# Kernel tuning notes

Measured on AMD Instinct MI355X. Metric: run time of the kernel, lower is better.

## Reference

```python
import jax, jax.numpy as jnp
import numpy as np
import math

EMBED_DIM = 768
NUM_HEADS = 12
MLP_HIDDEN = int(EMBED_DIM * 2.0)
LN_EPS = 1e-6


def _complex_linear(r, i, wr, wi, br, bi):
    # (r + i*j) @ (wr + wi*j)^T + (br + bi*j)
    out_r = r @ wr.T - i @ wi.T + br
    out_i = r @ wi.T + i @ wr.T + bi
    return out_r, out_i


def _complex_layernorm(r, i, gamma, beta):
    # magnitude-based LN over feature dim; gamma/beta: [F, 2]
    mag = jnp.sqrt(r * r + i * i + LN_EPS)           # [..., F]
    mean = mag.mean(axis=-1, keepdims=True)
    var = ((mag - mean) ** 2).mean(axis=-1, keepdims=True)  # unbiased=False
    norm_mag = (mag - mean) / jnp.sqrt(var + LN_EPS)
    scale = norm_mag / (mag + LN_EPS)
    r_n = r * scale
    i_n = i * scale
    return gamma[..., 0] * r_n + beta[..., 0], gamma[..., 1] * i_n + beta[..., 1]


def setup_inputs() -> dict:
    key = jax.random.key(0)
    ks = jax.random.split(key, 12)
    B, N, E, H = 2, 2048, EMBED_DIM, MLP_HIDDEN
    std_qkv = math.sqrt(2.0 / (E + 3 * E))
    std_proj = math.sqrt(2.0 / (E + E))
    std_fc1 = math.sqrt(2.0 / (E + H))
    std_fc2 = math.sqrt(2.0 / (H + E))
    inp = {
        "x": jax.random.normal(ks[0], (B, N, 2 * E), dtype=jnp.float32),
        "norm1_gamma": 1.0 + 0.1 * jax.random.normal(ks[1], (E, 2), dtype=jnp.float32),
        "norm1_beta": 0.1 * jax.random.normal(ks[2], (E, 2), dtype=jnp.float32),
        "qkv_wr": std_qkv * jax.random.normal(ks[3], (3 * E, E), dtype=jnp.float32),
        "qkv_wi": std_qkv * jax.random.normal(ks[4], (3 * E, E), dtype=jnp.float32),
        "qkv_br": jnp.zeros((3 * E,), dtype=jnp.float32),
        "qkv_bi": jnp.zeros((3 * E,), dtype=jnp.float32),
        "proj_wr": std_proj * jax.random.normal(ks[5], (E, E), dtype=jnp.float32),
        "proj_wi": std_proj * jax.random.normal(ks[6], (E, E), dtype=jnp.float32),
        "proj_br": jnp.zeros((E,), dtype=jnp.float32),
        "proj_bi": jnp.zeros((E,), dtype=jnp.float32),
        "norm2_gamma": 1.0 + 0.1 * jax.random.normal(ks[7], (E, 2), dtype=jnp.float32),
        "norm2_beta": 0.1 * jax.random.normal(ks[8], (E, 2), dtype=jnp.float32),
        "fc1_wr": std_fc1 * jax.random.normal(ks[9], (H, E), dtype=jnp.float32),
        "fc1_wi": std_fc1 * jax.random.normal(ks[10], (H, E), dtype=jnp.float32),
        "fc1_br": jnp.zeros((H,), dtype=jnp.float32),
        "fc1_bi": jnp.zeros((H,), dtype=jnp.float32),
        "fc2_wr": std_fc2 * jax.random.normal(ks[11], (E, H), dtype=jnp.float32),
        "fc2_wi": std_fc2 * jax.random.normal(jax.random.fold_in(key, 99), (E, H), dtype=jnp.float32),
        "fc2_br": jnp.zeros((E,), dtype=jnp.float32),
        "fc2_bi": jnp.zeros((E,), dtype=jnp.float32),
    }
    return inp


def reference(x, norm1_gamma, norm1_beta, qkv_wr, qkv_wi, qkv_br, qkv_bi,
              proj_wr, proj_wi, proj_br, proj_bi, norm2_gamma, norm2_beta,
              fc1_wr, fc1_wi, fc1_br, fc1_bi, fc2_wr, fc2_wi, fc2_br, fc2_bi):
    B, N, _ = x.shape
    E, nH = EMBED_DIM, NUM_HEADS
    hd = E // nH
    xc = x.reshape(B, N, E, 2)
    xr, xi = xc[..., 0], xc[..., 1]

    # --- attention branch ---
    nr, ni = _complex_layernorm(xr, xi, norm1_gamma, norm1_beta)
    qkv_r, qkv_i = _complex_linear(nr, ni, qkv_wr, qkv_wi, qkv_br, qkv_bi)  # [B,N,3E]
    # split to [3, B, nH, N, hd]
    def split_heads(t):
        return t.reshape(B, N, 3, nH, hd).transpose(2, 0, 3, 1, 4)
    qkv_r = split_heads(qkv_r)
    qkv_i = split_heads(qkv_i)
    qr, kr, vr = qkv_r[0], qkv_r[1], qkv_r[2]
    qi, ki, vi = qkv_i[0], qkv_i[1], qkv_i[2]

    # complex attention scores: q * conj-free formulation per source
    attn_real = jnp.einsum('bhqd,bhkd->bhqk', qr, kr) + jnp.einsum('bhqd,bhkd->bhqk', qi, ki)
    attn_imag = jnp.einsum('bhqd,bhkd->bhqk', qr, ki) - jnp.einsum('bhqd,bhkd->bhqk', qi, kr)
    attn_mag = jnp.sqrt(attn_real ** 2 + attn_imag ** 2 + 1e-8) / math.sqrt(hd)
    attn_w = jax.nn.softmax(attn_mag, axis=-1)
    out_r = jnp.einsum('bhqk,bhkd->bhqd', attn_w, vr)
    out_i = jnp.einsum('bhqk,bhkd->bhqd', attn_w, vi)
    # [B,nH,N,hd] -> [B,N,E]
    out_r = out_r.transpose(0, 2, 1, 3).reshape(B, N, E)
    out_i = out_i.transpose(0, 2, 1, 3).reshape(B, N, E)
    pr, pi = _complex_linear(out_r, out_i, proj_wr, proj_wi, proj_br, proj_bi)
    xr = xr + pr
    xi = xi + pi

    # --- MLP branch ---
    nr2, ni2 = _complex_layernorm(xr, xi, norm2_gamma, norm2_beta)
    h_r, h_i = _complex_linear(nr2, ni2, fc1_wr, fc1_wi, fc1_br, fc1_bi)
    h_r = jax.nn.gelu(h_r, approximate=False)
    h_i = jax.nn.gelu(h_i, approximate=False)
    m_r, m_i = _complex_linear(h_r, h_i, fc2_wr, fc2_wi, fc2_br, fc2_bi)
    xr = xr + m_r
    xi = xi + m_i

    return jnp.stack([xr, xi], axis=-1).reshape(B, N, 2 * E)
```

## Files before the change

### kernel.cpp

```cpp
#include <hip/hip_runtime.h>
#include <cmath>

typedef __bf16 bf16;
typedef __bf16 bf16x8 __attribute__((ext_vector_type(8)));
typedef __bf16 bf16x4 __attribute__((ext_vector_type(4)));
typedef float  f32x4  __attribute__((ext_vector_type(4)));
typedef unsigned int u32x4 __attribute__((ext_vector_type(4)));

#define MFMA16(a, b, c) __builtin_amdgcn_mfma_f32_16x16x32_bf16((a), (b), (c), 0, 0, 0)
#define LOG2E 1.44269504088896f

static __device__ __forceinline__ void gl_lds16(const void* g, void* l) {
    __builtin_amdgcn_global_load_lds((const __attribute__((address_space(1))) void*)g,
                                     (__attribute__((address_space(3))) void*)l, 16, 0, 0);
}

static __device__ __forceinline__ bf16x8 bneg8(bf16x8 x) {
    u32x4 u = __builtin_bit_cast(u32x4, x);
    u = u ^ 0x80008000u;
    return __builtin_bit_cast(bf16x8, u);
}

static __device__ __forceinline__ f32x4 zero4() {
    return f32x4{0.0f, 0.0f, 0.0f, 0.0f};
}

__global__ void fill_kernel(float* p, float v, int n) {
    for (int i = blockIdx.x * blockDim.x + threadIdx.x; i < n; i += gridDim.x * blockDim.x)
        p[i] = v;
}

struct Cvt8 {
    const float* s[8];
    bf16* d[8];
    int boff[9];
};
__global__ __launch_bounds__(256) void cvt8_kernel(Cvt8 c) {
    int blk = blockIdx.x;
    int seg = 0;
#pragma unroll
    for (int k = 0; k < 7; ++k)
        if (blk >= c.boff[k + 1]) seg = k + 1;
    const int local = blk - c.boff[seg];
    const int i = local * 1024 + threadIdx.x * 4;
    const float4 v = *(const float4*)(c.s[seg] + i);
    bf16x4 o;
    o[0] = (bf16)v.x; o[1] = (bf16)v.y; o[2] = (bf16)v.z; o[3] = (bf16)v.w;
    *(bf16x4*)(c.d[seg] + i) = o;
}

template <bool ILV>
__global__ __launch_bounds__(256) void cln_kernel(
    const float* __restrict__ xa, const float* __restrict__ xb,
    const float* __restrict__ gamma, const float* __restrict__ beta,
    bf16* __restrict__ nr, bf16* __restrict__ ni) {
    __shared__ float red[4];
    const int t = threadIdx.x;
    const size_t base = (size_t)blockIdx.x * 768;

    float r[3], im[3], mg[3];
#pragma unroll
    for (int j = 0; j < 3; ++j) {
        const int f = t + j * 256;
        if (ILV) {
            const float2 v = ((const float2*)xa)[base + f];
            r[j] = v.x;
            im[j] = v.y;
        } else {
            r[j] = xa[base + f];
            im[j] = xb[base + f];
        }
        mg[j] = __builtin_amdgcn_sqrtf(r[j] * r[j] + im[j] * im[j] + 1e-6f);
    }
    float s = mg[0] + mg[1] + mg[2];
#pragma unroll
    for (int m = 32; m >= 1; m >>= 1) s += __shfl_xor(s, m);
    if ((t & 63) == 0) red[t >> 6] = s;
    __syncthreads();
    const float mean = (red[0] + red[1] + red[2] + red[3]) * (1.0f / 768.0f);
    __syncthreads();

    float v2 = 0.0f;
#pragma unroll
    for (int j = 0; j < 3; ++j) {
        const float d = mg[j] - mean;
        v2 += d * d;
    }
#pragma unroll
    for (int m = 32; m >= 1; m >>= 1) v2 += __shfl_xor(v2, m);
    if ((t & 63) == 0) red[t >> 6] = v2;
    __syncthreads();
    const float var = (red[0] + red[1] + red[2] + red[3]) * (1.0f / 768.0f);
    const float rstd = rsqrtf(var + 1e-6f);

#pragma unroll
    for (int j = 0; j < 3; ++j) {
        const int f = t + j * 256;
        const float sc = (mg[j] - mean) * rstd / (mg[j] + 1e-6f);
        nr[base + f] = (bf16)(gamma[2 * f] * (r[j] * sc) + beta[2 * f]);
        ni[base + f] = (bf16)(gamma[2 * f + 1] * (im[j] * sc) + beta[2 * f + 1]);
    }
}

template <int BM, int BN, int MODE, int OCC>
__global__ __launch_bounds__(256, OCC) void cgemm_kernel(
    const bf16* __restrict__ Ar, const bf16* __restrict__ Ai,
    const bf16* __restrict__ Wr, const bf16* __restrict__ Wi,
    const float* __restrict__ br, const float* __restrict__ bi,
    const float* __restrict__ resr, const float* __restrict__ resi,
    float* __restrict__ outFr, float* __restrict__ outFi,
    bf16* __restrict__ outBr, bf16* __restrict__ outBi,
    int N, int K) {
    constexpr int MR = BM / 32;
    constexpr int NR = BN / 32;
    constexpr int ASEG = BM / 8;
    constexpr int NSEG = (BM + BN) / 8;
    constexpr int SPW = NSEG / 4;

    __shared__ __align__(16) bf16 sA[2][BM][64];
    __shared__ __align__(16) bf16 sB[2][BN][64];

    const int tid = threadIdx.x;
    const int wave = tid >> 6, lane = tid & 63;
    const int lg = lane >> 4, lr = lane & 15;

    const int nwgx = gridDim.x;
    int wg = blockIdx.y * nwgx + blockIdx.x;
    const int cpx = (nwgx * gridDim.y) >> 3;
    wg = (wg & 7) * cpx + (wg >> 3);
    const int row0 = (wg % nwgx) * BM, col0 = (wg / nwgx) * BN;

    const int wm = (wave >> 1) * (BM / 2), wn = (wave & 1) * (BN / 2);

    const int srow = lane >> 3;
    const int schunk = (lane & 7) ^ srow;
    const int spl = schunk >> 2;
    const int sc8 = (schunk & 3) * 8;

    auto issue = [&](int buf, int kt) {
#pragma unroll
        for (int s = 0; s < SPW; ++s) {
            const int id = wave * SPW + s;
            if (id < ASEG) {
                const int row = id * 8 + srow;
                gl_lds16((spl ? Ai : Ar) + (size_t)(row0 + row) * K + kt + sc8,
                         &sA[buf][id * 8][0]);
            } else {
                const int row = (id - ASEG) * 8 + srow;
                gl_lds16((spl ? Wi : Wr) + (size_t)(col0 + row) * K + kt + sc8,
                         &sB[buf][(id - ASEG) * 8][0]);
            }
        }
    };

    f32x4 accr[MR][NR], acci[MR][NR];
#pragma unroll
    for (int a = 0; a < MR; ++a)
#pragma unroll
        for (int b2 = 0; b2 < NR; ++b2) {
            accr[a][b2] = zero4();
            acci[a][b2] = zero4();
        }

    issue(0, 0);

    const int KT = K / 32;
    for (int kt = 0; kt < KT; ++kt) {
        const int buf = kt & 1;
        if (kt + 1 < KT) {
            issue(buf ^ 1, (kt + 1) * 32);
            __builtin_amdgcn_sched_barrier(0);
            if constexpr (SPW == 8)
                asm volatile("s_waitcnt vmcnt(8)" ::: "memory");
            else if constexpr (SPW == 6)
                asm volatile("s_waitcnt vmcnt(6)" ::: "memory");
            else
                asm volatile("s_waitcnt vmcnt(0)" ::: "memory");
        } else {
            asm volatile("s_waitcnt vmcnt(0)" ::: "memory");
        }
        __builtin_amdgcn_sched_barrier(0);
        __builtin_amdgcn_s_barrier();
        __builtin_amdgcn_sched_barrier(0);

        bf16x8 ar[MR], ai[MR], an[MR];
#pragma unroll
        for (int mt = 0; mt < MR; ++mt) {
            const int rr = wm + mt * 16 + lr;
            const int slr = lg ^ (rr & 7);
            const int sli = (4 + lg) ^ (rr & 7);
            ar[mt] = *(const bf16x8*)(&sA[buf][rr][slr * 8]);
            ai[mt] = *(const bf16x8*)(&sA[buf][rr][sli * 8]);
            an[mt] = bneg8(ai[mt]);
        }
#pragma unroll
        for (int nt = 0; nt < NR; ++nt) {
            const int rr = wn + nt * 16 + lr;
            const int slr = lg ^ (rr & 7);
            const int sli = (4 + lg) ^ (rr & 7);
            const bf16x8 br8 = *(const bf16x8*)(&sB[buf][rr][slr * 8]);
            const bf16x8 bi8 = *(const bf16x8*)(&sB[buf][rr][sli * 8]);
#pragma unroll
            for (int mt = 0; mt < MR; ++mt) {
                accr[mt][nt] = MFMA16(ar[mt], br8, accr[mt][nt]);
                accr[mt][nt] = MFMA16(an[mt], bi8, accr[mt][nt]);
                acci[mt][nt] = MFMA16(ar[mt], bi8, acci[mt][nt]);
                acci[mt][nt] = MFMA16(ai[mt], br8, acci[mt][nt]);
            }
        }
    }

#pragma unroll
    for (int nt = 0; nt < NR; ++nt) {
        const int col = col0 + wn + nt * 16 + lr;
        const float bre = br[col], bie = bi[col];
#pragma unroll
        for (int mt = 0; mt < MR; ++mt) {
#pragma unroll
            for (int j = 0; j < 4; ++j) {
                const int row = row0 + wm + mt * 16 + lg * 4 + j;
                float vr = accr[mt][nt][j] + bre;
                float vi = acci[mt][nt][j] + bie;
                const size_t o = (size_t)row * N + col;
                if (MODE == 0) {
                    outBr[o] = (bf16)vr;
                    outBi[o] = (bf16)vi;
                } else if (MODE == 1) {
                    const float2 rv = ((const float2*)resr)[(size_t)row * 768 + col];
                    outFr[o] = rv.x + vr;
                    outFi[o] = rv.y + vi;
                } else if (MODE == 2) {
                    const float t2r = fmaf(vr * vr, 0.044715f, 1.0f);
                    const float er = __builtin_amdgcn_exp2f(vr * t2r * 2.3022082f);
                    vr = vr - vr * __builtin_amdgcn_rcpf(er + 1.0f);
                    const float t2i = fmaf(vi * vi, 0.044715f, 1.0f);
                    const float ei = __builtin_amdgcn_exp2f(vi * t2i * 2.3022082f);
                    vi = vi - vi * __builtin_amdgcn_rcpf(ei + 1.0f);
                    outBr[o] = (bf16)vr;
                    outBi[o] = (bf16)vi;
                } else {
                    const size_t ro = (size_t)row * 768 + col;
                    outFr[(size_t)row * 1536 + 2 * col]     = resr[ro] + vr;
                    outFr[(size_t)row * 1536 + 2 * col + 1] = resi[ro] + vi;
                }
            }
        }
    }
}

__global__ __launch_bounds__(256) void vtrans_kernel(
    const bf16* __restrict__ qkvr, const bf16* __restrict__ qkvi,
    bf16* __restrict__ vtr, bf16* __restrict__ vti) {
    __shared__ bf16 sr[64][65];
    __shared__ bf16 si[64][65];
    const int t = threadIdx.x;
    const int nb = blockIdx.x, h = blockIdx.y, b = blockIdx.z;
    const size_t ld = 2304;
    const bf16* srcr = qkvr + (size_t)(b * 2048 + nb * 64) * ld + 1536 + h * 64;
    const bf16* srci = qkvi + (size_t)(b * 2048 + nb * 64) * ld + 1536 + h * 64;
#pragma unroll
    for (int j = 0; j < 16; ++j) {
        const int idx = t + 256 * j;
        const int n = idx >> 6, d = idx & 63;
        sr[n][d] = srcr[(size_t)n * ld + d];
        si[n][d] = srci[(size_t)n * ld + d];
    }
    __syncthreads();
    bf16* dstr = vtr + (size_t)(b * 12 + h) * 64 * 2048 + nb * 64;
    bf16* dsti = vti + (size_t)(b * 12 + h) * 64 * 2048 + nb * 64;
#pragma unroll
    for (int j = 0; j < 16; ++j) {
        const int idx = t + 256 * j;
        const int d = idx >> 6, n = idx & 63;
        dstr[(size_t)d * 2048 + n] = sr[n][d];
        dsti[(size_t)d * 2048 + n] = si[n][d];
    }
}

__global__ __launch_bounds__(256, 3) void cattn_kernel(
    const bf16* __restrict__ qkvr, const bf16* __restrict__ qkvi,
    const bf16* __restrict__ vtr, const bf16* __restrict__ vti,
    bf16* __restrict__ aor, bf16* __restrict__ aoi) {
    __shared__ __align__(16) bf16 sK[2][2][32][64];
    __shared__ __align__(16) bf16 sV[3][64][64];
    __shared__ __align__(16) bf16 sP[4][16][40];

    const int tid = threadIdx.x;
    const int w = tid >> 6, lane = tid & 63;
    const int lg = lane >> 4, lr = lane & 15;
    const int qb = blockIdx.x, h = blockIdx.y, b = blockIdx.z;
    const int ld = 2304;

    const int s_krow = lane >> 3;
    const int s_kch8 = ((lane & 7) ^ s_krow) * 8;
    const int s_vlog = (lane & 7) ^ s_krow;
    const int s_vpl = s_vlog >> 2;
    const int s_vk8 = (s_vlog & 3) * 8;

    const bf16* kbase0 = qkvr + (size_t)b * 2048 * ld + 768 + h * 64;
    const bf16* kbase1 = qkvi + (size_t)b * 2048 * ld + 768 + h * 64;
    const bf16* vbase = (s_vpl ? vti : vtr) + (size_t)(b * 12 + h) * 64 * 2048;

    const bf16* kp0 = kbase0 + (size_t)(w * 8 + s_krow) * ld + s_kch8;
    const bf16* kp1 = kbase1 + (size_t)(w * 8 + s_krow) * ld + s_kch8;
    const bf16* vp0 = vbase + (size_t)(w * 8 + s_krow) * 2048 + s_vk8;
    const bf16* vp1 = vbase + (size_t)((4 + w) * 8 + s_krow) * 2048 + s_vk8;

    auto stage = [&](int kb, int vs) {
        gl_lds16(kp0, &sK[kb][0][w * 8][0]);
        gl_lds16(kp1, &sK[kb][1][w * 8][0]);
        gl_lds16(vp0, &sV[vs][w * 8][0]);
        gl_lds16(vp1, &sV[vs][(4 + w) * 8][0]);
        kp0 += 32 * ld;
        kp1 += 32 * ld;
        vp0 += 32;
        vp1 += 32;
    };

    stage(0, 0);

    const size_t qoff = (size_t)(b * 2048 + qb * 64 + w * 16 + lr) * ld + h * 64;
    bf16x8 aqr[2], aqi[2];
#pragma unroll
    for (int ks = 0; ks < 2; ++ks) {
        aqr[ks] = *(const bf16x8*)(qkvr + qoff + ks * 32 + lg * 8);
        aqi[ks] = *(const bf16x8*)(qkvi + qoff + ks * 32 + lg * 8);
    }

    f32x4 our[4], oui[4];
#pragma unroll
    for (int d = 0; d < 4; ++d) {
        our[d] = zero4();
        oui[d] = zero4();
    }
    const float C1 = 0.125f * LOG2E;
    float mrun = -1e30f;
    float lrun_p = 0.0f;
    float thr2 = -1.0f;
    float mC2 = 0.0f;

    bf16x8 pfPrev = __builtin_bit_cast(bf16x8, u32x4{0u, 0u, 0u, 0u});
    int vcur = 0, vlast = 0;
    const int slr = lg ^ (lr & 7);
    const int sli = (4 + lg) ^ (lr & 7);

    for (int kt = 0; kt < 64; ++kt) {
        const int kcur = kt & 1;
        int vnext = vcur + 1;
        if (vnext == 3) vnext = 0;
        if (kt < 63) {
            stage(kcur ^ 1, vnext);
            __builtin_amdgcn_sched_barrier(0);
            asm volatile("s_waitcnt vmcnt(4)" ::: "memory");
        } else {
            asm volatile("s_waitcnt vmcnt(0)" ::: "memory");
        }
        __builtin_amdgcn_sched_barrier(0);
        __builtin_amdgcn_s_barrier();
        __builtin_amdgcn_sched_barrier(0);

        f32x4 str[2], sti[2];
        str[0] = zero4(); str[1] = zero4();
        sti[0] = zero4(); sti[1] = zero4();
        __builtin_amdgcn_s_setprio(1);
#pragma unroll
        for (int t = 0; t < 2; ++t) {
#pragma unroll
            for (int ks = 0; ks < 2; ++ks) {
                const int ch = ((ks << 2) | lg) ^ (lr & 7);
                const bf16x8 kr8 = *(const bf16x8*)(&sK[kcur][0][t * 16 + lr][ch * 8]);
                const bf16x8 ki8 = *(const bf16x8*)(&sK[kcur][1][t * 16 + lr][ch * 8]);
                const bf16x8 kn8 = bneg8(kr8);
                str[t] = MFMA16(kr8, aqr[ks], str[t]);
                str[t] = MFMA16(ki8, aqi[ks], str[t]);
                sti[t] = MFMA16(ki8, aqr[ks], sti[t]);
                sti[t] = MFMA16(kn8, aqi[ks], sti[t]);
            }
        }
        if (kt > 0) {
#pragma unroll
            for (int d = 0; d < 4; ++d) {
                const bf16x8 vr8 = *(const bf16x8*)(&sV[vlast][d * 16 + lr][slr * 8]);
                const bf16x8 vi8 = *(const bf16x8*)(&sV[vlast][d * 16 + lr][sli * 8]);
                our[d] = MFMA16(pfPrev, vr8, our[d]);
                oui[d] = MFMA16(pfPrev, vi8, oui[d]);
            }
        }
        __builtin_amdgcn_s_setprio(0);

        float v[8];
        float vmax = 0.0f;
#pragma unroll
        for (int t = 0; t < 2; ++t)
#pragma unroll
            for (int j = 0; j < 4; ++j) {
                const float sr = str[t][j], si = sti[t][j];
                const float vv = fmaf(sr, sr, fmaf(si, si, 1e-8f));
                v[t * 4 + j] = vv;
                vmax = fmaxf(vmax, vv);
            }

        if (!__all(vmax <= thr2)) {
            vmax = fmaxf(vmax, __shfl_xor(vmax, 16));
            vmax = fmaxf(vmax, __shfl_xor(vmax, 32));
            const float tm = __builtin_amdgcn_sqrtf(vmax) * 0.125f;
            const float mnew = fmaxf(mrun, tm);
            const float corr = __builtin_amdgcn_exp2f((mrun - mnew) * LOG2E);
            float cj[4];
#pragma unroll
            for (int j = 0; j < 4; ++j) cj[j] = __shfl(corr, lg * 4 + j);
#pragma unroll
            for (int d = 0; d < 4; ++d)
#pragma unroll
                for (int j = 0; j < 4; ++j) {
                    our[d][j] *= cj[j];
                    oui[d][j] *= cj[j];
                }
            lrun_p *= corr;
            mrun = mnew;
            const float m8 = mrun + 8.0f;
            thr2 = 64.0f * m8 * m8;
            mC2 = -mrun * LOG2E;
        }

        float p[8];
        float ls = 0.0f;
#pragma unroll
        for (int i = 0; i < 8; ++i) {
            p[i] = __builtin_amdgcn_exp2f(
                fmaf(__builtin_amdgcn_sqrtf(v[i]), C1, mC2));
            ls += p[i];
        }
        lrun_p += ls;

#pragma unroll
        for (int t = 0; t < 2; ++t) {
            bf16x4 pk;
#pragma unroll
            for (int j = 0; j < 4; ++j) pk[j] = (bf16)p[t * 4 + j];
            *(bf16x4*)(&sP[w][lr][t * 16 + lg * 4]) = pk;
        }
        pfPrev = *(const bf16x8*)(&sP[w][lr][lg * 8]);

        vlast = vcur;
        vcur = vnext;
    }

#pragma unroll
    for (int d = 0; d < 4; ++d) {
        const bf16x8 vr8 = *(const bf16x8*)(&sV[vlast][d * 16 + lr][slr * 8]);
        const bf16x8 vi8 = *(const bf16x8*)(&sV[vlast][d * 16 + lr][sli * 8]);
        our[d] = MFMA16(pfPrev, vr8, our[d]);
        oui[d] = MFMA16(pfPrev, vi8, oui[d]);
    }

    float lsum = lrun_p;
    lsum += __shfl_xor(lsum, 16);
    lsum += __shfl_xor(lsum, 32);

    float linv[4];
#pragma unroll
    for (int j = 0; j < 4; ++j) {
        const float lj = __shfl(lsum, lg * 4 + j);
        linv[j] = __builtin_amdgcn_rcpf(lj);
    }
#pragma unroll
    for (int d = 0; d < 4; ++d)
#pragma unroll
        for (int j = 0; j < 4; ++j) {
            const int row = b * 2048 + qb * 64 + w * 16 + lg * 4 + j;
            const int col = h * 64 + d * 16 + lr;
            aor[(size_t)row * 768 + col] = (bf16)(our[d][j] * linv[j]);
            aoi[(size_t)row * 768 + col] = (bf16)(oui[d][j] * linv[j]);
        }
}

extern "C" void kernel_launch(void* const* d_in, const int* in_sizes, int n_in,
                              void* d_out, int out_size, void* d_ws, size_t ws_size,
                              hipStream_t stream) {
    const float* x      = (const float*)d_in[0];
    const float* n1g    = (const float*)d_in[1];
    const float* n1b    = (const float*)d_in[2];
    const float* qkvwr  = (const float*)d_in[3];
    const float* qkvwi  = (const float*)d_in[4];
    const float* qkvbr  = (const float*)d_in[5];
    const float* qkvbi  = (const float*)d_in[6];
    const float* projwr = (const float*)d_in[7];
    const float* projwi = (const float*)d_in[8];
    const float* projbr = (const float*)d_in[9];
    const float* projbi = (const float*)d_in[10];
    const float* n2g    = (const float*)d_in[11];
    const float* n2b    = (const float*)d_in[12];
    const float* fc1wr  = (const float*)d_in[13];
    const float* fc1wi  = (const float*)d_in[14];
    const float* fc1br  = (const float*)d_in[15];
    const float* fc1bi  = (const float*)d_in[16];
    const float* fc2wr  = (const float*)d_in[17];
    const float* fc2wi  = (const float*)d_in[18];
    const float* fc2br  = (const float*)d_in[19];
    const float* fc2bi  = (const float*)d_in[20];

    const int M = 4096, E = 768, E3 = 2304, HH = 1536;

    char* base = (char*)d_ws;
    size_t off = 0;
    auto alloc = [&](size_t bytes) -> void* {
        void* p = base + off;
        off += (bytes + 255) & ~(size_t)255;
        return p;
    };
    float* xr2 = (float*)alloc((size_t)M * E * 4);
    float* xi2 = (float*)alloc((size_t)M * E * 4);
    bf16* nr   = (bf16*)alloc((size_t)M * E * 2);
    bf16* ni   = (bf16*)alloc((size_t)M * E * 2);
    bf16* wqr  = (bf16*)alloc((size_t)E3 * E * 2);
    bf16* wqi  = (bf16*)alloc((size_t)E3 * E * 2);
    bf16* wpr  = (bf16*)alloc((size_t)E * E * 2);
    bf16* wpi  = (bf16*)alloc((size_t)E * E * 2);
    bf16* w1r  = (bf16*)alloc((size_t)HH * E * 2);
    bf16* w1i  = (bf16*)alloc((size_t)HH * E * 2);
    bf16* w2r  = (bf16*)alloc((size_t)E * HH * 2);
    bf16* w2i  = (bf16*)alloc((size_t)E * HH * 2);
    bf16* qkr  = (bf16*)alloc((size_t)M * E3 * 2);
    bf16* qki  = (bf16*)alloc((size_t)M * E3 * 2);
    bf16* vtr  = (bf16*)alloc((size_t)24 * 64 * 2048 * 2);
    bf16* vti  = (bf16*)alloc((size_t)24 * 64 * 2048 * 2);
    bf16* aor  = (bf16*)alloc((size_t)M * E * 2);
    bf16* aoi  = (bf16*)alloc((size_t)M * E * 2);
    bf16* hr   = (bf16*)alloc((size_t)M * HH * 2);
    bf16* hi   = (bf16*)alloc((size_t)M * HH * 2);

    if (off > ws_size) {
        fill_kernel<<<1024, 256, 0, stream>>>((float*)d_out, 1.0e9f, out_size);
        return;
    }

    Cvt8 c;
    c.s[0] = qkvwr; c.d[0] = wqr;
    c.s[1] = qkvwi; c.d[1] = wqi;
    c.s[2] = projwr; c.d[2] = wpr;
    c.s[3] = projwi; c.d[3] = wpi;
    c.s[4] = fc1wr; c.d[4] = w1r;
    c.s[5] = fc1wi; c.d[5] = w1i;
    c.s[6] = fc2wr; c.d[6] = w2r;
    c.s[7] = fc2wi; c.d[7] = w2i;
    const int nseg[8] = {E3 * E, E3 * E, E * E, E * E, HH * E, HH * E, E * HH, E * HH};
    int cum = 0;
    for (int k = 0; k < 8; ++k) {
        c.boff[k] = cum;
        cum += nseg[k] / 1024;
    }
    c.boff[8] = cum;
    cvt8_kernel<<<cum, 256, 0, stream>>>(c);

    cln_kernel<true><<<M, 256, 0, stream>>>(x, nullptr, n1g, n1b, nr, ni);
    cgemm_kernel<128, 128, 0, 2><<<dim3(32, 18), 256, 0, stream>>>(
        nr, ni, wqr, wqi, qkvbr, qkvbi, nullptr, nullptr, nullptr, nullptr,
        qkr, qki, E3, E);
    vtrans_kernel<<<dim3(32, 12, 2), 256, 0, stream>>>(qkr, qki, vtr, vti);
    cattn_kernel<<<dim3(32, 12, 2), 256, 0, stream>>>(qkr, qki, vtr, vti, aor, aoi);
    cgemm_kernel<128, 64, 1, 3><<<dim3(32, 12), 256, 0, stream>>>(
        aor, aoi, wpr, wpi, projbr, projbi, x, nullptr, xr2, xi2, nullptr, nullptr,
        E, E);
    cln_kernel<false><<<M, 256, 0, stream>>>(xr2, xi2, n2g, n2b, nr, ni);
    cgemm_kernel<128, 128, 2, 2><<<dim3(32, 12), 256, 0, stream>>>(
        nr, ni, w1r, w1i, fc1br, fc1bi, nullptr, nullptr, nullptr, nullptr,
        hr, hi, HH, E);
    cgemm_kernel<128, 64, 3, 3><<<dim3(32, 12), 256, 0, stream>>>(
        hr, hi, w2r, w2i, fc2br, fc2bi, xr2, xi2, (float*)d_out, nullptr,
        nullptr, nullptr, E, HH);
}
```

Baseline: 340.4 us.

## Produce transposed V directly from a swapped-operand GEMM, dropping the transpose kernel

The QKV projection is split in two. One GEMM writes only Q and K with a 1536-wide row stride. A new GEMM mode computes V transposed by swapping operands (W_v times X^T) and adds the bias per row, so the separate vtrans kernel and its extra global round trip go away. The attention kernel also precomputes a negated Q-imag fragment once instead of negating K for every tile. The QKV and fc1 GEMMs switch to 64x128 tiles to launch more blocks. The risk is that the transposed GEMM reads X as its B operand with a different access pattern, and there is one more GEMM launch.

```diff
diff --git a/kernel.cpp b/kernel.cpp
--- a/kernel.cpp
+++ b/kernel.cpp
@@ -213,16 +213,24 @@
 #pragma unroll
     for (int nt = 0; nt < NR; ++nt) {
         const int col = col0 + wn + nt * 16 + lr;
-        const float bre = br[col], bie = bi[col];
+        const float bre = (MODE == 4) ? 0.0f : br[col];
+        const float bie = (MODE == 4) ? 0.0f : bi[col];
 #pragma unroll
         for (int mt = 0; mt < MR; ++mt) {
 #pragma unroll
             for (int j = 0; j < 4; ++j) {
                 const int row = row0 + wm + mt * 16 + lg * 4 + j;
-                float vr = accr[mt][nt][j] + bre;
-                float vi = acci[mt][nt][j] + bie;
+                float vr = accr[mt][nt][j];
+                float vi = acci[mt][nt][j];
+                if (MODE == 4) {
+                    vr += br[row];
+                    vi += bi[row];
+                } else {
+                    vr += bre;
+                    vi += bie;
+                }
                 const size_t o = (size_t)row * N + col;
-                if (MODE == 0) {
+                if (MODE == 0 || MODE == 4) {
                     outBr[o] = (bf16)vr;
                     outBi[o] = (bf16)vi;
                 } else if (MODE == 1) {
@@ -248,37 +256,8 @@
     }
 }
 
-__global__ __launch_bounds__(256) void vtrans_kernel(
-    const bf16* __restrict__ qkvr, const bf16* __restrict__ qkvi,
-    bf16* __restrict__ vtr, bf16* __restrict__ vti) {
-    __shared__ bf16 sr[64][65];
-    __shared__ bf16 si[64][65];
-    const int t = threadIdx.x;
-    const int nb = blockIdx.x, h = blockIdx.y, b = blockIdx.z;
-    const size_t ld = 2304;
-    const bf16* srcr = qkvr + (size_t)(b * 2048 + nb * 64) * ld + 1536 + h * 64;
-    const bf16* srci = qkvi + (size_t)(b * 2048 + nb * 64) * ld + 1536 + h * 64;
-#pragma unroll
-    for (int j = 0; j < 16; ++j) {
-        const int idx = t + 256 * j;
-        const int n = idx >> 6, d = idx & 63;
-        sr[n][d] = srcr[(size_t)n * ld + d];
-        si[n][d] = srci[(size_t)n * ld + d];
-    }
-    __syncthreads();
-    bf16* dstr = vtr + (size_t)(b * 12 + h) * 64 * 2048 + nb * 64;
-    bf16* dsti = vti + (size_t)(b * 12 + h) * 64 * 2048 + nb * 64;
-#pragma unroll
-    for (int j = 0; j < 16; ++j) {
-        const int idx = t + 256 * j;
-        const int d = idx >> 6, n = idx & 63;
-        dstr[(size_t)d * 2048 + n] = sr[n][d];
-        dsti[(size_t)d * 2048 + n] = si[n][d];
-    }
-}
-
 __global__ __launch_bounds__(256, 3) void cattn_kernel(
-    const bf16* __restrict__ qkvr, const bf16* __restrict__ qkvi,
+    const bf16* __restrict__ qkr, const bf16* __restrict__ qki,
     const bf16* __restrict__ vtr, const bf16* __restrict__ vti,
     bf16* __restrict__ aor, bf16* __restrict__ aoi) {
     __shared__ __align__(16) bf16 sK[2][2][32][64];
@@ -289,7 +268,7 @@
     const int w = tid >> 6, lane = tid & 63;
     const int lg = lane >> 4, lr = lane & 15;
     const int qb = blockIdx.x, h = blockIdx.y, b = blockIdx.z;
-    const int ld = 2304;
+    const int ld = 1536;
 
     const int s_krow = lane >> 3;
     const int s_kch8 = ((lane & 7) ^ s_krow) * 8;
@@ -297,14 +276,14 @@
     const int s_vpl = s_vlog >> 2;
     const int s_vk8 = (s_vlog & 3) * 8;
 
-    const bf16* kbase0 = qkvr + (size_t)b * 2048 * ld + 768 + h * 64;
-    const bf16* kbase1 = qkvi + (size_t)b * 2048 * ld + 768 + h * 64;
-    const bf16* vbase = (s_vpl ? vti : vtr) + (size_t)(b * 12 + h) * 64 * 2048;
+    const bf16* kbase0 = qkr + (size_t)b * 2048 * ld + 768 + h * 64;
+    const bf16* kbase1 = qki + (size_t)b * 2048 * ld + 768 + h * 64;
+    const bf16* vbase = (s_vpl ? vti : vtr) + (size_t)(h * 64) * 4096 + b * 2048;
 
     const bf16* kp0 = kbase0 + (size_t)(w * 8 + s_krow) * ld + s_kch8;
     const bf16* kp1 = kbase1 + (size_t)(w * 8 + s_krow) * ld + s_kch8;
-    const bf16* vp0 = vbase + (size_t)(w * 8 + s_krow) * 2048 + s_vk8;
-    const bf16* vp1 = vbase + (size_t)((4 + w) * 8 + s_krow) * 2048 + s_vk8;
+    const bf16* vp0 = vbase + (size_t)(w * 8 + s_krow) * 4096 + s_vk8;
+    const bf16* vp1 = vbase + (size_t)((4 + w) * 8 + s_krow) * 4096 + s_vk8;
 
     auto stage = [&](int kb, int vs) {
         gl_lds16(kp0, &sK[kb][0][w * 8][0]);
@@ -320,11 +299,12 @@
     stage(0, 0);
 
     const size_t qoff = (size_t)(b * 2048 + qb * 64 + w * 16 + lr) * ld + h * 64;
-    bf16x8 aqr[2], aqi[2];
+    bf16x8 aqr[2], aqi[2], aqin[2];
 #pragma unroll
     for (int ks = 0; ks < 2; ++ks) {
-        aqr[ks] = *(const bf16x8*)(qkvr + qoff + ks * 32 + lg * 8);
-        aqi[ks] = *(const bf16x8*)(qkvi + qoff + ks * 32 + lg * 8);
+        aqr[ks] = *(const bf16x8*)(qkr + qoff + ks * 32 + lg * 8);
+        aqi[ks] = *(const bf16x8*)(qki + qoff + ks * 32 + lg * 8);
+        aqin[ks] = bneg8(aqi[ks]);
     }
 
     f32x4 our[4], oui[4];
@@ -370,11 +350,10 @@
                 const int ch = ((ks << 2) | lg) ^ (lr & 7);
                 const bf16x8 kr8 = *(const bf16x8*)(&sK[kcur][0][t * 16 + lr][ch * 8]);
                 const bf16x8 ki8 = *(const bf16x8*)(&sK[kcur][1][t * 16 + lr][ch * 8]);
-                const bf16x8 kn8 = bneg8(kr8);
                 str[t] = MFMA16(kr8, aqr[ks], str[t]);
                 str[t] = MFMA16(ki8, aqi[ks], str[t]);
                 sti[t] = MFMA16(ki8, aqr[ks], sti[t]);
-                sti[t] = MFMA16(kn8, aqi[ks], sti[t]);
+                sti[t] = MFMA16(kr8, aqin[ks], sti[t]);
             }
         }
         if (kt > 0) {
@@ -521,10 +500,10 @@
     bf16* w1i  = (bf16*)alloc((size_t)HH * E * 2);
     bf16* w2r  = (bf16*)alloc((size_t)E * HH * 2);
     bf16* w2i  = (bf16*)alloc((size_t)E * HH * 2);
-    bf16* qkr  = (bf16*)alloc((size_t)M * E3 * 2);
-    bf16* qki  = (bf16*)alloc((size_t)M * E3 * 2);
-    bf16* vtr  = (bf16*)alloc((size_t)24 * 64 * 2048 * 2);
-    bf16* vti  = (bf16*)alloc((size_t)24 * 64 * 2048 * 2);
+    bf16* qkr  = (bf16*)alloc((size_t)M * HH * 2);
+    bf16* qki  = (bf16*)alloc((size_t)M * HH * 2);
+    bf16* vtr  = (bf16*)alloc((size_t)E * M * 2);
+    bf16* vti  = (bf16*)alloc((size_t)E * M * 2);
     bf16* aor  = (bf16*)alloc((size_t)M * E * 2);
     bf16* aoi  = (bf16*)alloc((size_t)M * E * 2);
     bf16* hr   = (bf16*)alloc((size_t)M * HH * 2);
@@ -554,16 +533,19 @@
     cvt8_kernel<<<cum, 256, 0, stream>>>(c);
 
     cln_kernel<true><<<M, 256, 0, stream>>>(x, nullptr, n1g, n1b, nr, ni);
-    cgemm_kernel<128, 128, 0, 2><<<dim3(32, 18), 256, 0, stream>>>(
+    cgemm_kernel<64, 128, 0, 3><<<dim3(64, 12), 256, 0, stream>>>(
         nr, ni, wqr, wqi, qkvbr, qkvbi, nullptr, nullptr, nullptr, nullptr,
-        qkr, qki, E3, E);
-    vtrans_kernel<<<dim3(32, 12, 2), 256, 0, stream>>>(qkr, qki, vtr, vti);
+        qkr, qki, HH, E);
+    cgemm_kernel<64, 128, 4, 3><<<dim3(12, 32), 256, 0, stream>>>(
+        wqr + (size_t)HH * E, wqi + (size_t)HH * E, nr, ni,
+        qkvbr + HH, qkvbi + HH, nullptr, nullptr, nullptr, nullptr,
+        vtr, vti, M, E);
     cattn_kernel<<<dim3(32, 12, 2), 256, 0, stream>>>(qkr, qki, vtr, vti, aor, aoi);
     cgemm_kernel<128, 64, 1, 3><<<dim3(32, 12), 256, 0, stream>>>(
         aor, aoi, wpr, wpi, projbr, projbi, x, nullptr, xr2, xi2, nullptr, nullptr,
         E, E);
     cln_kernel<false><<<M, 256, 0, stream>>>(xr2, xi2, n2g, n2b, nr, ni);
-    cgemm_kernel<128, 128, 2, 2><<<dim3(32, 12), 256, 0, stream>>>(
+    cgemm_kernel<64, 128, 2, 3><<<dim3(64, 12), 256, 0, stream>>>(
         nr, ni, w1r, w1i, fc1br, fc1bi, nullptr, nullptr, nullptr, nullptr,
         hr, hi, HH, E);
     cgemm_kernel<128, 64, 3, 3><<<dim3(32, 12), 256, 0, stream>>>(
```

Result: no change. 334.2 us (-1.8%).
